# Performance work log

Hardware: AMD Instinct MI355X
Metric: run time of the kernel (lower is better)

The kernel has to match this reference:

```python
import jax, jax.numpy as jnp
import numpy as np

BN_EPS = 1e-5
LEAKY_SLOPE = 0.01

def setup_inputs() -> dict:
    key = jax.random.key(0)
    ks = jax.random.split(key, 8)
    B, N, C, D = 8, 2048, 128, 32  # batch, points, inchannels, outchannels
    s = 0.05
    return {
        "x": jax.random.normal(ks[0], (B, N, C), dtype=jnp.float32),
        "Wq": jax.random.normal(ks[1], (D, C), dtype=jnp.float32) * s,
        "Wk": jax.random.normal(ks[2], (D, C), dtype=jnp.float32) * s,
        "Wv": jax.random.normal(ks[3], (C, C), dtype=jnp.float32) * s,
        "Wp": jax.random.normal(ks[4], (C, C), dtype=jnp.float32) * s,
        "bn_gamma": jnp.ones((C,), dtype=jnp.float32),
        "bn_beta": jnp.zeros((C,), dtype=jnp.float32),
        "bn_mean": jax.random.normal(ks[5], (C,), dtype=jnp.float32) * 0.01,
        "bn_var": jnp.abs(jax.random.normal(ks[6], (C,), dtype=jnp.float32)) * 0.1 + 0.9,
    }

def reference(x, Wq, Wk, Wv, Wp, bn_gamma, bn_beta, bn_mean, bn_var):
    # x: [B, N, C]; 1x1 Conv1d == per-point linear map
    q = jnp.einsum('bnc,dc->bnd', x, Wq)          # [B, N, D]
    k = jnp.einsum('bnc,dc->bnd', x, Wk)          # [B, N, D]
    v = jnp.einsum('bnc,oc->bno', x, Wv)          # [B, N, C]
    energy = jnp.einsum('bnd,bmd->bnm', q, k)     # [B, Nq, Nk]
    # offset-attention: softmax over the QUERY axis (dim=1), then L1-renorm over keys
    attn = jax.nn.softmax(energy, axis=1)
    attn = attn / (1e-9 + attn.sum(axis=-1, keepdims=True))
    x_r = jnp.einsum('bnm,bmc->bnc', attn, v)     # [B, N, C]
    # project(x - x_r): 1x1 conv + BatchNorm (eval, running stats) + LeakyReLU; dropout p=0
    d = x - x_r
    y = jnp.einsum('bnc,oc->bno', d, Wp)
    y = (y - bn_mean) * (bn_gamma / jnp.sqrt(bn_var + BN_EPS)) + bn_beta
    y = jnp.where(y >= 0, y, LEAKY_SLOPE * y)
    return y + x
```

## Files before the change

### kernel.cpp

```cpp
#include <hip/hip_runtime.h>
#include <stdint.h>

#define BB 8
#define NN 2048
#define CC 128
#define DD 32
#define LOG2E 1.44269504088896340736f

typedef __attribute__((ext_vector_type(8))) short short8;
typedef __attribute__((ext_vector_type(4))) short short4v;
typedef __attribute__((ext_vector_type(4))) float f32x4;

#define MFMA(a,b,c) __builtin_amdgcn_mfma_f32_16x16x32_bf16(a,b,c,0,0,0)

__device__ __forceinline__ short f2b(float f){
  uint32_t u = __float_as_uint(f);
  uint32_t r = (u + 0x7fffu + ((u >> 16) & 1u)) >> 16;
  return (short)r;
}
__device__ __forceinline__ float b2f(short s){
  uint32_t u = ((uint32_t)(uint16_t)s) << 16;
  return __uint_as_float(u);
}

__global__ void k_pack(const float* __restrict__ Wq, const float* __restrict__ Wk,
                       const float* __restrict__ Wv, const float* __restrict__ Wp,
                       const float* __restrict__ g, const float* __restrict__ bt,
                       const float* __restrict__ mu, const float* __restrict__ vr,
                       short* __restrict__ wqkv, short* __restrict__ wp,
                       float* __restrict__ scale, float* __restrict__ shift){
  int i = blockIdx.x*256 + threadIdx.x;
  if (i < 192*128){
    int r = i >> 7, c = i & 127;
    float w = (r < 32) ? Wq[r*128+c] : (r < 64) ? Wk[(r-32)*128+c] : Wv[(r-64)*128+c];
    wqkv[i] = f2b(w);
  }
  if (i < 128*128) wp[i] = f2b(Wp[i]);
  if (i < 128){
    float s = g[i] * rsqrtf(vr[i] + 1e-5f);
    scale[i] = s;
    shift[i] = bt[i] - mu[i]*s;
  }
}

__global__ __launch_bounds__(256,4) void k_qkv(const float* __restrict__ x, const short* __restrict__ wqkv,
    short* __restrict__ qb, short* __restrict__ kb, short* __restrict__ vt){
  const int tid = threadIdx.x;
  const int wv = tid >> 6, l = tid & 63, lrow = l & 15, lg = l >> 4;
  const int r0 = blockIdx.x*16;
  const int base = wv*3;
  const float* xr = x + (long)(r0 + lrow)*CC;
  short8 a[4];
  #pragma unroll
  for (int ks=0; ks<4; ks++){
    f32x4 u0 = *(const f32x4*)(xr + ks*32 + lg*8);
    f32x4 u1 = *(const f32x4*)(xr + ks*32 + lg*8 + 4);
    short8 t;
    #pragma unroll
    for (int j=0;j<4;j++){ t[j] = f2b(u0[j]); t[4+j] = f2b(u1[j]); }
    a[ks] = t;
  }
  f32x4 acc[3];
  #pragma unroll
  for (int i=0;i<3;i++) acc[i] = f32x4{0.f,0.f,0.f,0.f};
  #pragma unroll
  for (int of=0; of<3; of++){
    #pragma unroll
    for (int ks=0; ks<4; ks++){
      short8 bfr = *(const short8*)(wqkv + ((base+of)*16 + lrow)*CC + ks*32 + lg*8);
      acc[of] = MFMA(a[ks], bfr, acc[of]);
    }
  }
  const int b = r0 / NN, nin = r0 % NN;
  #pragma unroll
  for (int of=0; of<3; of++){
    const int oo = base + of;
    const int o = oo*16 + lrow;
    if (oo < 2){
      #pragma unroll
      for (int rr=0; rr<4; rr++) qb[(long)(r0 + lg*4 + rr)*DD + o] = f2b(acc[of][rr]*LOG2E);
    } else if (oo < 4){
      #pragma unroll
      for (int rr=0; rr<4; rr++) kb[(long)(r0 + lg*4 + rr)*DD + (o-32)] = f2b(acc[of][rr]);
    } else {
      short4v s;
      #pragma unroll
      for (int rr=0; rr<4; rr++) s[rr] = f2b(acc[of][rr]);
      *(short4v*)(vt + (long)(b*CC + (o-64))*NN + nin + lg*4) = s;
    }
  }
}

__global__ __launch_bounds__(256,4) void k_colsum(const short* __restrict__ qb, const short* __restrict__ kb,
                                                  float* __restrict__ csum){
  const int tid = threadIdx.x;
  const int wv = tid >> 6, l = tid & 63, lrow = l & 15, lg = l >> 4;
  const int bq = blockIdx.x & 31;
  const int b = bq >> 2, q = bq & 3;
  const int m0 = (blockIdx.x >> 5)*64 + wv*16;
  short8 afr = *(const short8*)(kb + (long)(b*NN + m0 + lrow)*DD + lg*8);
  const short* qbase = qb + (long)b*NN*DD;
  float sum[4] = {0.f,0.f,0.f,0.f};
  f32x4 z = {0.f,0.f,0.f,0.f};
  const int nbeg = q*512, nend = nbeg + 512;
  #pragma unroll 4
  for (int n0=nbeg; n0<nend; n0+=16){
    short8 bfr = *(const short8*)(qbase + (long)(n0 + lrow)*DD + lg*8);
    f32x4 e = MFMA(afr, bfr, z);
    #pragma unroll
    for (int r=0;r<4;r++) sum[r] += exp2f(e[r]);
  }
  #pragma unroll
  for (int mask=1; mask<16; mask<<=1){
    #pragma unroll
    for (int r=0;r<4;r++) sum[r] += __shfl_xor(sum[r], mask);
  }
  if (lrow == 0){
    #pragma unroll
    for (int r=0;r<4;r++) csum[q*(BB*NN) + b*NN + m0 + lg*4 + r] = sum[r];
  }
}

__global__ __launch_bounds__(256,2) void k_attn(const short* __restrict__ qb,
    const short* __restrict__ kb, const short* __restrict__ vt, const float* __restrict__ csum,
    short* __restrict__ accPb, float* __restrict__ Lp){
  __shared__ __align__(16) short lds[22016];
  const int tid = threadIdx.x;
  const int wv = tid >> 6, l = tid & 63, lrow = l & 15, lg = l >> 4;
  const int bq = blockIdx.x & 31;
  const int b = bq >> 2;
  const int quarter = bq & 3;
  const int rt = blockIdx.x >> 5;
  const int n0 = rt*128 + wv*32;
  const short* kbb = kb + (long)b*NN*DD;
  const short* vtb = vt + (long)b*CC*NN;
  float* sinvl = (float*)(lds + 20992);

  short8 qfr[2];
  #pragma unroll
  for (int rg=0; rg<2; rg++)
    qfr[rg] = *(const short8*)(qb + (long)(b*NN + n0 + rg*16 + lrow)*DD + lg*8);

  const int mbase = quarter*512;
  {
    const float* c0p = csum + b*NN + mbase;
    #pragma unroll
    for (int i=tid; i<512; i+=256){
      float s = c0p[i] + c0p[i + BB*NN] + c0p[i + 2*BB*NN] + c0p[i + 3*BB*NN];
      sinvl[i] = __builtin_amdgcn_rcpf(s);
    }
  }

  f32x4 acc[2][8];
  #pragma unroll
  for (int rg=0; rg<2; rg++)
    #pragma unroll
    for (int i=0;i<8;i++) acc[rg][i] = f32x4{0.f,0.f,0.f,0.f};
  float L[2][4] = {{0.f,0.f,0.f,0.f},{0.f,0.f,0.f,0.f}};

  short8 sv[4]; short8 sk[2];
  const int cr = tid >> 1, hf = tid & 1;
  auto loadT = [&](int m0){
    const short* s = vtb + (long)cr*NN + m0 + hf*32;
    sv[0] = *(const short8*)(s);
    sv[1] = *(const short8*)(s+8);
    sv[2] = *(const short8*)(s+16);
    sv[3] = *(const short8*)(s+24);
    if (tid < 128){
      const short* s2 = kbb + (long)(m0 + cr)*DD + hf*16;
      sk[0] = *(const short8*)(s2);
      sk[1] = *(const short8*)(s2+8);
    }
  };
  auto storeT = [&](){
    *(short8*)(lds + cr*72 + hf*32 + 0)  = sv[0];
    *(short8*)(lds + cr*72 + hf*32 + 8)  = sv[1];
    *(short8*)(lds + cr*72 + hf*32 + 16) = sv[2];
    *(short8*)(lds + cr*72 + hf*32 + 24) = sv[3];
    if (tid < 128){
      short* kb_t = lds + 9216;
      *(short8*)(kb_t + cr*40 + hf*16 + 0) = sk[0];
      *(short8*)(kb_t + cr*40 + hf*16 + 8) = sk[1];
    }
  };

  loadT(mbase);
  storeT();
  __syncthreads();

  short* pl = lds + 11776 + wv*2304;
  f32x4 z = {0.f,0.f,0.f,0.f};
  for (int it=0; it<8; it++){
    if (it < 7) loadT(mbase + it*64 + 64);
    short* kb_t = lds + 9216;
    short8 kf[4];
    #pragma unroll
    for (int mt=0; mt<4; mt++)
      kf[mt] = *(short8*)(kb_t + (mt*16 + lrow)*40 + lg*8);
    #pragma unroll
    for (int rg=0; rg<2; rg++){
      #pragma unroll
      for (int mt=0; mt<4; mt++){
        f32x4 e = MFMA(qfr[rg], kf[mt], z);
        float si = sinvl[it*64 + mt*16 + lrow];
        float p0 = exp2f(e[0])*si, p1 = exp2f(e[1])*si;
        float p2 = exp2f(e[2])*si, p3 = exp2f(e[3])*si;
        L[rg][0] += p0; L[rg][1] += p1; L[rg][2] += p2; L[rg][3] += p3;
        pl[(rg*16 + lg*4 + 0)*72 + mt*16 + lrow] = f2b(p0);
        pl[(rg*16 + lg*4 + 1)*72 + mt*16 + lrow] = f2b(p1);
        pl[(rg*16 + lg*4 + 2)*72 + mt*16 + lrow] = f2b(p2);
        pl[(rg*16 + lg*4 + 3)*72 + mt*16 + lrow] = f2b(p3);
      }
    }
    __builtin_amdgcn_s_setprio(1);
    #pragma unroll
    for (int ks=0; ks<2; ks++){
      short8 pa0 = *(short8*)(pl + (lrow)*72 + ks*32 + lg*8);
      short8 pa1 = *(short8*)(pl + (16 + lrow)*72 + ks*32 + lg*8);
      #pragma unroll
      for (int cf=0; cf<8; cf++){
        short8 vb_ = *(short8*)(lds + (cf*16 + lrow)*72 + ks*32 + lg*8);
        acc[0][cf] = MFMA(pa0, vb_, acc[0][cf]);
        acc[1][cf] = MFMA(pa1, vb_, acc[1][cf]);
      }
    }
    __builtin_amdgcn_s_setprio(0);
    __syncthreads();
    if (it < 7){
      storeT();
      __syncthreads();
    }
  }

  #pragma unroll
  for (int mask=1; mask<16; mask<<=1){
    #pragma unroll
    for (int rg=0; rg<2; rg++)
      #pragma unroll
      for (int r=0;r<4;r++) L[rg][r] += __shfl_xor(L[rg][r], mask);
  }
  const long tile = (long)((b*16 + rt)*4 + quarter);
  if (lrow == 0){
    #pragma unroll
    for (int rg=0; rg<2; rg++)
      #pragma unroll
      for (int r=0;r<4;r++)
        Lp[tile*128 + wv*32 + rg*16 + lg*4 + r] = L[rg][r];
  }

  short* aP = accPb + tile*128*128;
  #pragma unroll
  for (int rg=0; rg<2; rg++)
    #pragma unroll
    for (int cf=0; cf<8; cf++)
      #pragma unroll
      for (int r=0;r<4;r++)
        aP[(wv*32 + rg*16 + lg*4 + r)*128 + cf*16 + lrow] = f2b(acc[rg][cf][r]);
}

__global__ __launch_bounds__(256,4) void k_fin(const float* __restrict__ x, const short* __restrict__ accPb,
    const float* __restrict__ Lp, const short* __restrict__ wp, const float* __restrict__ scale,
    const float* __restrict__ shift, float* __restrict__ out){
  __shared__ __align__(16) short dl[16*136];
  __shared__ float linv_s[16];
  const int tid = threadIdx.x;
  const int wv = tid >> 6, l = tid & 63, lrow = l & 15, lg = l >> 4;
  const int b = blockIdx.x >> 7;
  const int rt = blockIdx.x & 127;
  const int nb = rt*16;
  const long tileIdx = (long)(b*16 + (rt>>3))*4;
  const int rowoff = (rt&7)*16;

  if (tid < 16){
    float Ls = Lp[(tileIdx+0)*128 + rowoff + tid] + Lp[(tileIdx+1)*128 + rowoff + tid]
             + Lp[(tileIdx+2)*128 + rowoff + tid] + Lp[(tileIdx+3)*128 + rowoff + tid];
    linv_s[tid] = __builtin_amdgcn_rcpf(1e-9f + Ls);
  }

  const int row_l = tid >> 4;
  const int c0 = (tid & 15)*8;
  float a[8];
  #pragma unroll
  for (int j=0;j<8;j++) a[j] = 0.f;
  #pragma unroll
  for (int p=0;p<4;p++){
    short8 v = *(const short8*)(accPb + (tileIdx+p)*128*128 + (rowoff+row_l)*128 + c0);
    #pragma unroll
    for (int j=0;j<8;j++) a[j] += b2f(v[j]);
  }
  const float* xr = x + ((long)(b*NN + nb + row_l))*CC + c0;
  f32x4 x0 = *(const f32x4*)(xr);
  f32x4 x1 = *(const f32x4*)(xr + 4);
  __syncthreads();
  {
    const float li = linv_s[row_l];
    short4v d0, d1;
    #pragma unroll
    for (int j=0;j<4;j++){
      d0[j] = f2b(x0[j] - a[j]*li);
      d1[j] = f2b(x1[j] - a[4+j]*li);
    }
    *(short4v*)(dl + row_l*136 + c0) = d0;
    *(short4v*)(dl + row_l*136 + c0 + 4) = d1;
  }
  __syncthreads();

  f32x4 yac[2];
  yac[0] = f32x4{0.f,0.f,0.f,0.f};
  yac[1] = f32x4{0.f,0.f,0.f,0.f};
  #pragma unroll
  for (int ks=0; ks<4; ks++){
    short8 da = *(short8*)(dl + lrow*136 + ks*32 + lg*8);
    #pragma unroll
    for (int of=0; of<2; of++){
      short8 wfr = *(const short8*)(wp + ((wv*2+of)*16 + lrow)*CC + ks*32 + lg*8);
      yac[of] = MFMA(da, wfr, yac[of]);
    }
  }
  float* ob = out + ((long)(b*NN + nb))*CC;
  const float* xb = x + ((long)(b*NN + nb))*CC;
  #pragma unroll
  for (int of=0; of<2; of++){
    const int o = (wv*2+of)*16 + lrow;
    const float sc = scale[o], sh = shift[o];
    #pragma unroll
    for (int r=0;r<4;r++){
      float y = yac[of][r]*sc + sh;
      y = (y >= 0.f) ? y : 0.01f*y;
      ob[(lg*4+r)*CC + o] = y + xb[(lg*4+r)*CC + o];
    }
  }
}

extern "C" void kernel_launch(void* const* d_in, const int* in_sizes, int n_in,
                              void* d_out, int out_size, void* d_ws, size_t ws_size,
                              hipStream_t stream) {
  const float* x  = (const float*)d_in[0];
  const float* Wq = (const float*)d_in[1];
  const float* Wk = (const float*)d_in[2];
  const float* Wv = (const float*)d_in[3];
  const float* Wp = (const float*)d_in[4];
  const float* g  = (const float*)d_in[5];
  const float* bt = (const float*)d_in[6];
  const float* mu = (const float*)d_in[7];
  const float* vr = (const float*)d_in[8];
  float* out = (float*)d_out;

  char* ws = (char*)d_ws;
  short* wqkv  = (short*)(ws + 0);
  short* wp    = (short*)(ws + 49152);
  float* scale = (float*)(ws + 81920);
  float* shift = (float*)(ws + 82432);
  short* qb    = (short*)(ws + 98304);
  short* kb    = (short*)(ws + 1146880);
  short* vt    = (short*)(ws + 2195456);
  float* csum  = (float*)(ws + 6389760);
  float* Lp    = (float*)(ws + 6651904);
  short* accPb = (short*)(ws + 6914048);

  k_pack<<<96, 256, 0, stream>>>(Wq, Wk, Wv, Wp, g, bt, mu, vr, wqkv, wp, scale, shift);
  k_qkv<<<1024, 256, 0, stream>>>(x, wqkv, qb, kb, vt);
  k_colsum<<<1024, 256, 0, stream>>>(qb, kb, csum);
  k_attn<<<512, 256, 0, stream>>>(qb, kb, vt, csum, accPb, Lp);
  k_fin<<<1024, 256, 0, stream>>>(x, accPb, Lp, wp, scale, shift, out);
}
```

Baseline: 131.9 us.

## Fuse weight packing into QKV and final projection into attention via last-block counter

Drops the separate weight-pack kernel: k_qkv now loads fp32 Wq/Wk/Wv and converts them to bf16 inline, and the final stage builds the BN scale/shift and bf16 Wp fragments on the fly. The final projection kernel is folded into k_attn. A per-row-tile atomic counter, reset in k_colsum, picks the last of the four quarter blocks to finish, and that block reduces the partial accumulators and applies the projection, BatchNorm and LeakyReLU for 128 rows. This removes two kernel launches and their gaps. In exchange, weight conversion is repeated in every block, and the tail work runs on only a quarter of the attention blocks, which serialises it behind the last finisher.

```diff
diff --git a/kernel.cpp b/kernel.cpp
--- a/kernel.cpp
+++ b/kernel.cpp
@@ -23,27 +23,8 @@
   return __uint_as_float(u);
 }
 
-__global__ void k_pack(const float* __restrict__ Wq, const float* __restrict__ Wk,
-                       const float* __restrict__ Wv, const float* __restrict__ Wp,
-                       const float* __restrict__ g, const float* __restrict__ bt,
-                       const float* __restrict__ mu, const float* __restrict__ vr,
-                       short* __restrict__ wqkv, short* __restrict__ wp,
-                       float* __restrict__ scale, float* __restrict__ shift){
-  int i = blockIdx.x*256 + threadIdx.x;
-  if (i < 192*128){
-    int r = i >> 7, c = i & 127;
-    float w = (r < 32) ? Wq[r*128+c] : (r < 64) ? Wk[(r-32)*128+c] : Wv[(r-64)*128+c];
-    wqkv[i] = f2b(w);
-  }
-  if (i < 128*128) wp[i] = f2b(Wp[i]);
-  if (i < 128){
-    float s = g[i] * rsqrtf(vr[i] + 1e-5f);
-    scale[i] = s;
-    shift[i] = bt[i] - mu[i]*s;
-  }
-}
-
-__global__ __launch_bounds__(256,4) void k_qkv(const float* __restrict__ x, const short* __restrict__ wqkv,
+__global__ __launch_bounds__(256,4) void k_qkv(const float* __restrict__ x,
+    const float* __restrict__ Wq, const float* __restrict__ Wk, const float* __restrict__ Wv,
     short* __restrict__ qb, short* __restrict__ kb, short* __restrict__ vt){
   const int tid = threadIdx.x;
   const int wv = tid >> 6, l = tid & 63, lrow = l & 15, lg = l >> 4;
@@ -65,9 +46,16 @@
   for (int i=0;i<3;i++) acc[i] = f32x4{0.f,0.f,0.f,0.f};
   #pragma unroll
   for (int of=0; of<3; of++){
+    const int oo = base + of;
+    const int row = oo*16 + lrow;
+    const float* Wr = (oo < 2) ? (Wq + row*CC) : (oo < 4) ? (Wk + (row-32)*CC) : (Wv + (row-64)*CC);
     #pragma unroll
     for (int ks=0; ks<4; ks++){
-      short8 bfr = *(const short8*)(wqkv + ((base+of)*16 + lrow)*CC + ks*32 + lg*8);
+      f32x4 w0 = *(const f32x4*)(Wr + ks*32 + lg*8);
+      f32x4 w1 = *(const f32x4*)(Wr + ks*32 + lg*8 + 4);
+      short8 bfr;
+      #pragma unroll
+      for (int j=0;j<4;j++){ bfr[j] = f2b(w0[j]); bfr[4+j] = f2b(w1[j]); }
       acc[of] = MFMA(a[ks], bfr, acc[of]);
     }
   }
@@ -92,9 +80,10 @@
 }
 
 __global__ __launch_bounds__(256,4) void k_colsum(const short* __restrict__ qb, const short* __restrict__ kb,
-                                                  float* __restrict__ csum){
+                                                  float* __restrict__ csum, int* __restrict__ cnt){
   const int tid = threadIdx.x;
   const int wv = tid >> 6, l = tid & 63, lrow = l & 15, lg = l >> 4;
+  if (blockIdx.x == 0 && tid < 128) cnt[tid] = 0;
   const int bq = blockIdx.x & 31;
   const int b = bq >> 2, q = bq & 3;
   const int m0 = (blockIdx.x >> 5)*64 + wv*16;
@@ -121,9 +110,12 @@
   }
 }
 
-__global__ __launch_bounds__(256,2) void k_attn(const short* __restrict__ qb,
+__global__ __launch_bounds__(256,2) void k_attn(const float* __restrict__ x, const short* __restrict__ qb,
     const short* __restrict__ kb, const short* __restrict__ vt, const float* __restrict__ csum,
-    short* __restrict__ accPb, float* __restrict__ Lp){
+    const float* __restrict__ Wp, const float* __restrict__ g, const float* __restrict__ bt,
+    const float* __restrict__ mu, const float* __restrict__ vr,
+    short* __restrict__ accPb, float* __restrict__ Lp, int* __restrict__ cnt,
+    float* __restrict__ out){
   __shared__ __align__(16) short lds[22016];
   const int tid = threadIdx.x;
   const int wv = tid >> 6, l = tid & 63, lrow = l & 15, lg = l >> 4;
@@ -239,7 +231,8 @@
       #pragma unroll
       for (int r=0;r<4;r++) L[rg][r] += __shfl_xor(L[rg][r], mask);
   }
-  const long tile = (long)((b*16 + rt)*4 + quarter);
+  const long t4 = (long)(b*16 + rt)*4;
+  const long tile = t4 + quarter;
   if (lrow == 0){
     #pragma unroll
     for (int rg=0; rg<2; rg++)
@@ -256,78 +249,92 @@
       #pragma unroll
       for (int r=0;r<4;r++)
         aP[(wv*32 + rg*16 + lg*4 + r)*128 + cf*16 + lrow] = f2b(acc[rg][cf][r]);
-}
-
-__global__ __launch_bounds__(256,4) void k_fin(const float* __restrict__ x, const short* __restrict__ accPb,
-    const float* __restrict__ Lp, const short* __restrict__ wp, const float* __restrict__ scale,
-    const float* __restrict__ shift, float* __restrict__ out){
-  __shared__ __align__(16) short dl[16*136];
-  __shared__ float linv_s[16];
-  const int tid = threadIdx.x;
-  const int wv = tid >> 6, l = tid & 63, lrow = l & 15, lg = l >> 4;
-  const int b = blockIdx.x >> 7;
-  const int rt = blockIdx.x & 127;
-  const int nb = rt*16;
-  const long tileIdx = (long)(b*16 + (rt>>3))*4;
-  const int rowoff = (rt&7)*16;
-
-  if (tid < 16){
-    float Ls = Lp[(tileIdx+0)*128 + rowoff + tid] + Lp[(tileIdx+1)*128 + rowoff + tid]
-             + Lp[(tileIdx+2)*128 + rowoff + tid] + Lp[(tileIdx+3)*128 + rowoff + tid];
-    linv_s[tid] = __builtin_amdgcn_rcpf(1e-9f + Ls);
-  }
-
-  const int row_l = tid >> 4;
-  const int c0 = (tid & 15)*8;
-  float a[8];
-  #pragma unroll
-  for (int j=0;j<8;j++) a[j] = 0.f;
-  #pragma unroll
-  for (int p=0;p<4;p++){
-    short8 v = *(const short8*)(accPb + (tileIdx+p)*128*128 + (rowoff+row_l)*128 + c0);
-    #pragma unroll
-    for (int j=0;j<8;j++) a[j] += b2f(v[j]);
-  }
-  const float* xr = x + ((long)(b*NN + nb + row_l))*CC + c0;
-  f32x4 x0 = *(const f32x4*)(xr);
-  f32x4 x1 = *(const f32x4*)(xr + 4);
+
+  __threadfence();
+  __syncthreads();
+  int* flagp = (int*)(lds + 21504);
+  if (tid == 0)
+    *flagp = (atomicAdd(&cnt[b*16 + rt], 1) == 3) ? 1 : 0;
+  __syncthreads();
+  if (!*flagp) return;
+  __threadfence();
+
+  float* linvl = (float*)(lds + 20992);
+  short* dl = lds;
+  if (tid < 128){
+    float Ls = Lp[t4*128 + tid] + Lp[(t4+1)*128 + tid]
+             + Lp[(t4+2)*128 + tid] + Lp[(t4+3)*128 + tid];
+    linvl[tid] = __builtin_amdgcn_rcpf(1e-9f + Ls);
+  }
   __syncthreads();
   {
-    const float li = linv_s[row_l];
-    short4v d0, d1;
-    #pragma unroll
-    for (int j=0;j<4;j++){
-      d0[j] = f2b(x0[j] - a[j]*li);
-      d1[j] = f2b(x1[j] - a[4+j]*li);
-    }
-    *(short4v*)(dl + row_l*136 + c0) = d0;
-    *(short4v*)(dl + row_l*136 + c0 + 4) = d1;
-  }
-  __syncthreads();
-
-  f32x4 yac[2];
-  yac[0] = f32x4{0.f,0.f,0.f,0.f};
-  yac[1] = f32x4{0.f,0.f,0.f,0.f};
-  #pragma unroll
-  for (int ks=0; ks<4; ks++){
-    short8 da = *(short8*)(dl + lrow*136 + ks*32 + lg*8);
-    #pragma unroll
-    for (int of=0; of<2; of++){
-      short8 wfr = *(const short8*)(wp + ((wv*2+of)*16 + lrow)*CC + ks*32 + lg*8);
-      yac[of] = MFMA(da, wfr, yac[of]);
-    }
-  }
-  float* ob = out + ((long)(b*NN + nb))*CC;
-  const float* xb = x + ((long)(b*NN + nb))*CC;
+    const int row = tid >> 1, half = tid & 1;
+    const float li = linvl[row];
+    const float* xr2 = x + ((long)(b*NN + rt*128 + row))*CC + half*64;
+    const short* ap0 = accPb + t4*128*128 + row*128 + half*64;
+    #pragma unroll
+    for (int c8=0; c8<8; c8++){
+      float s[8];
+      #pragma unroll
+      for (int j=0;j<8;j++) s[j] = 0.f;
+      #pragma unroll
+      for (int q2=0; q2<4; q2++){
+        short8 v = *(const short8*)(ap0 + q2*128*128 + c8*8);
+        #pragma unroll
+        for (int j=0;j<8;j++) s[j] += b2f(v[j]);
+      }
+      f32x4 x0 = *(const f32x4*)(xr2 + c8*8);
+      f32x4 x1 = *(const f32x4*)(xr2 + c8*8 + 4);
+      short8 d8;
+      #pragma unroll
+      for (int j=0;j<4;j++){
+        d8[j]   = f2b(x0[j] - s[j]*li);
+        d8[4+j] = f2b(x1[j] - s[4+j]*li);
+      }
+      *(short8*)(dl + row*136 + half*64 + c8*8) = d8;
+    }
+  }
+  __syncthreads();
+
+  short8 wfr[2][4];
+  float sc[2], sh[2];
   #pragma unroll
   for (int of=0; of<2; of++){
     const int o = (wv*2+of)*16 + lrow;
-    const float sc = scale[o], sh = shift[o];
-    #pragma unroll
-    for (int r=0;r<4;r++){
-      float y = yac[of][r]*sc + sh;
-      y = (y >= 0.f) ? y : 0.01f*y;
-      ob[(lg*4+r)*CC + o] = y + xb[(lg*4+r)*CC + o];
+    #pragma unroll
+    for (int ks=0; ks<4; ks++){
+      const float* wr = Wp + o*CC + ks*32 + lg*8;
+      f32x4 w0 = *(const f32x4*)(wr);
+      f32x4 w1 = *(const f32x4*)(wr + 4);
+      #pragma unroll
+      for (int j=0;j<4;j++){ wfr[of][ks][j] = f2b(w0[j]); wfr[of][ks][4+j] = f2b(w1[j]); }
+    }
+    sc[of] = g[o] * rsqrtf(vr[o] + 1e-5f);
+    sh[of] = bt[o] - mu[o]*sc[of];
+  }
+  float* ob = out + ((long)(b*NN + rt*128))*CC;
+  const float* xb = x + ((long)(b*NN + rt*128))*CC;
+  #pragma unroll
+  for (int rb=0; rb<8; rb++){
+    f32x4 yac0 = f32x4{0.f,0.f,0.f,0.f};
+    f32x4 yac1 = f32x4{0.f,0.f,0.f,0.f};
+    #pragma unroll
+    for (int ks=0; ks<4; ks++){
+      short8 da = *(short8*)(dl + (rb*16 + lrow)*136 + ks*32 + lg*8);
+      yac0 = MFMA(da, wfr[0][ks], yac0);
+      yac1 = MFMA(da, wfr[1][ks], yac1);
+    }
+    #pragma unroll
+    for (int of=0; of<2; of++){
+      const f32x4 ya = of ? yac1 : yac0;
+      const int o = (wv*2+of)*16 + lrow;
+      #pragma unroll
+      for (int r=0;r<4;r++){
+        const int row = rb*16 + lg*4 + r;
+        float y = ya[r]*sc[of] + sh[of];
+        y = (y >= 0.f) ? y : 0.01f*y;
+        ob[(long)row*CC + o] = y + xb[(long)row*CC + o];
+      }
     }
   }
 }
@@ -347,20 +354,15 @@
   float* out = (float*)d_out;
 
   char* ws = (char*)d_ws;
-  short* wqkv  = (short*)(ws + 0);
-  short* wp    = (short*)(ws + 49152);
-  float* scale = (float*)(ws + 81920);
-  float* shift = (float*)(ws + 82432);
   short* qb    = (short*)(ws + 98304);
   short* kb    = (short*)(ws + 1146880);
   short* vt    = (short*)(ws + 2195456);
   float* csum  = (float*)(ws + 6389760);
   float* Lp    = (float*)(ws + 6651904);
   short* accPb = (short*)(ws + 6914048);
-
-  k_pack<<<96, 256, 0, stream>>>(Wq, Wk, Wv, Wp, g, bt, mu, vr, wqkv, wp, scale, shift);
-  k_qkv<<<1024, 256, 0, stream>>>(x, wqkv, qb, kb, vt);
-  k_colsum<<<1024, 256, 0, stream>>>(qb, kb, csum);
-  k_attn<<<512, 256, 0, stream>>>(qb, kb, vt, csum, accPb, Lp);
-  k_fin<<<1024, 256, 0, stream>>>(x, accPb, Lp, wp, scale, shift, out);
-}
+  int*   cnt   = (int*)(ws + 23691264);
+
+  k_qkv<<<1024, 256, 0, stream>>>(x, Wq, Wk, Wv, qb, kb, vt);
+  k_colsum<<<1024, 256, 0, stream>>>(qb, kb, csum, cnt);
+  k_attn<<<512, 256, 0, stream>>>(x, qb, kb, vt, csum, Wp, g, bt, mu, vr, accPb, Lp, cnt, out);
+}
```

Result: slower. 248.0 us (+88.1%).

## Double-buffer attention LDS tiles and fold weight packing into consumer kernels

Applied to the files above, without the earlier changes.

The k_pack launch is removed. k_qkv and k_fin now read the fp32 weights directly and convert them to bf16 in registers, and k_fin computes the BatchNorm scale and shift inline. This saves one kernel launch at the cost of redundant conversions in every block. In k_attn, the V/K tiles are double-buffered in LDS so the next tile is stored while the current one is consumed, which drops one __syncthreads per iteration. The extra LDS (about 67KB per block) may reduce occupancy.

```diff
diff --git a/kernel.cpp b/kernel.cpp
--- a/kernel.cpp
+++ b/kernel.cpp
@@ -23,27 +23,8 @@
   return __uint_as_float(u);
 }
 
-__global__ void k_pack(const float* __restrict__ Wq, const float* __restrict__ Wk,
-                       const float* __restrict__ Wv, const float* __restrict__ Wp,
-                       const float* __restrict__ g, const float* __restrict__ bt,
-                       const float* __restrict__ mu, const float* __restrict__ vr,
-                       short* __restrict__ wqkv, short* __restrict__ wp,
-                       float* __restrict__ scale, float* __restrict__ shift){
-  int i = blockIdx.x*256 + threadIdx.x;
-  if (i < 192*128){
-    int r = i >> 7, c = i & 127;
-    float w = (r < 32) ? Wq[r*128+c] : (r < 64) ? Wk[(r-32)*128+c] : Wv[(r-64)*128+c];
-    wqkv[i] = f2b(w);
-  }
-  if (i < 128*128) wp[i] = f2b(Wp[i]);
-  if (i < 128){
-    float s = g[i] * rsqrtf(vr[i] + 1e-5f);
-    scale[i] = s;
-    shift[i] = bt[i] - mu[i]*s;
-  }
-}
-
-__global__ __launch_bounds__(256,4) void k_qkv(const float* __restrict__ x, const short* __restrict__ wqkv,
+__global__ __launch_bounds__(256,4) void k_qkv(const float* __restrict__ x,
+    const float* __restrict__ Wq, const float* __restrict__ Wk, const float* __restrict__ Wv,
     short* __restrict__ qb, short* __restrict__ kb, short* __restrict__ vt){
   const int tid = threadIdx.x;
   const int wv = tid >> 6, l = tid & 63, lrow = l & 15, lg = l >> 4;
@@ -65,9 +46,16 @@
   for (int i=0;i<3;i++) acc[i] = f32x4{0.f,0.f,0.f,0.f};
   #pragma unroll
   for (int of=0; of<3; of++){
+    const int oo = base + of;
+    const int row = oo*16 + lrow;
+    const float* Wr = (oo < 2) ? (Wq + row*CC) : (oo < 4) ? (Wk + (row-32)*CC) : (Wv + (row-64)*CC);
     #pragma unroll
     for (int ks=0; ks<4; ks++){
-      short8 bfr = *(const short8*)(wqkv + ((base+of)*16 + lrow)*CC + ks*32 + lg*8);
+      f32x4 w0 = *(const f32x4*)(Wr + ks*32 + lg*8);
+      f32x4 w1 = *(const f32x4*)(Wr + ks*32 + lg*8 + 4);
+      short8 bfr;
+      #pragma unroll
+      for (int j=0;j<4;j++){ bfr[j] = f2b(w0[j]); bfr[4+j] = f2b(w1[j]); }
       acc[of] = MFMA(a[ks], bfr, acc[of]);
     }
   }
@@ -124,7 +112,7 @@
 __global__ __launch_bounds__(256,2) void k_attn(const short* __restrict__ qb,
     const short* __restrict__ kb, const short* __restrict__ vt, const float* __restrict__ csum,
     short* __restrict__ accPb, float* __restrict__ Lp){
-  __shared__ __align__(16) short lds[22016];
+  __shared__ __align__(16) short lds[33792];
   const int tid = threadIdx.x;
   const int wv = tid >> 6, l = tid & 63, lrow = l & 15, lg = l >> 4;
   const int bq = blockIdx.x & 31;
@@ -134,7 +122,7 @@
   const int n0 = rt*128 + wv*32;
   const short* kbb = kb + (long)b*NN*DD;
   const short* vtb = vt + (long)b*CC*NN;
-  float* sinvl = (float*)(lds + 20992);
+  float* sinvl = (float*)(lds + 32768);
 
   short8 qfr[2];
   #pragma unroll
@@ -172,27 +160,30 @@
       sk[1] = *(const short8*)(s2+8);
     }
   };
-  auto storeT = [&](){
-    *(short8*)(lds + cr*72 + hf*32 + 0)  = sv[0];
-    *(short8*)(lds + cr*72 + hf*32 + 8)  = sv[1];
-    *(short8*)(lds + cr*72 + hf*32 + 16) = sv[2];
-    *(short8*)(lds + cr*72 + hf*32 + 24) = sv[3];
+  auto storeT = [&](int buf){
+    short* base = lds + buf*11776;
+    *(short8*)(base + cr*72 + hf*32 + 0)  = sv[0];
+    *(short8*)(base + cr*72 + hf*32 + 8)  = sv[1];
+    *(short8*)(base + cr*72 + hf*32 + 16) = sv[2];
+    *(short8*)(base + cr*72 + hf*32 + 24) = sv[3];
     if (tid < 128){
-      short* kb_t = lds + 9216;
+      short* kb_t = base + 9216;
       *(short8*)(kb_t + cr*40 + hf*16 + 0) = sk[0];
       *(short8*)(kb_t + cr*40 + hf*16 + 8) = sk[1];
     }
   };
 
   loadT(mbase);
-  storeT();
+  storeT(0);
   __syncthreads();
 
-  short* pl = lds + 11776 + wv*2304;
+  short* pl = lds + 23552 + wv*2304;
   f32x4 z = {0.f,0.f,0.f,0.f};
   for (int it=0; it<8; it++){
+    const int cur = it & 1;
     if (it < 7) loadT(mbase + it*64 + 64);
-    short* kb_t = lds + 9216;
+    short* vt_t = lds + cur*11776;
+    short* kb_t = vt_t + 9216;
     short8 kf[4];
     #pragma unroll
     for (int mt=0; mt<4; mt++)
@@ -219,17 +210,14 @@
       short8 pa1 = *(short8*)(pl + (16 + lrow)*72 + ks*32 + lg*8);
       #pragma unroll
       for (int cf=0; cf<8; cf++){
-        short8 vb_ = *(short8*)(lds + (cf*16 + lrow)*72 + ks*32 + lg*8);
+        short8 vb_ = *(short8*)(vt_t + (cf*16 + lrow)*72 + ks*32 + lg*8);
         acc[0][cf] = MFMA(pa0, vb_, acc[0][cf]);
         acc[1][cf] = MFMA(pa1, vb_, acc[1][cf]);
       }
     }
     __builtin_amdgcn_s_setprio(0);
+    if (it < 7) storeT(cur ^ 1);
     __syncthreads();
-    if (it < 7){
-      storeT();
-      __syncthreads();
-    }
   }
 
   #pragma unroll
@@ -239,7 +227,7 @@
       #pragma unroll
       for (int r=0;r<4;r++) L[rg][r] += __shfl_xor(L[rg][r], mask);
   }
-  const long tile = (long)((b*16 + rt)*4 + quarter);
+  const long tile = (long)(b*16 + rt)*4 + quarter;
   if (lrow == 0){
     #pragma unroll
     for (int rg=0; rg<2; rg++)
@@ -259,17 +247,18 @@
 }
 
 __global__ __launch_bounds__(256,4) void k_fin(const float* __restrict__ x, const short* __restrict__ accPb,
-    const float* __restrict__ Lp, const short* __restrict__ wp, const float* __restrict__ scale,
-    const float* __restrict__ shift, float* __restrict__ out){
+    const float* __restrict__ Lp, const float* __restrict__ Wp, const float* __restrict__ g,
+    const float* __restrict__ bt, const float* __restrict__ mu, const float* __restrict__ vr,
+    float* __restrict__ out){
   __shared__ __align__(16) short dl[16*136];
   __shared__ float linv_s[16];
   const int tid = threadIdx.x;
   const int wv = tid >> 6, l = tid & 63, lrow = l & 15, lg = l >> 4;
   const int b = blockIdx.x >> 7;
-  const int rt = blockIdx.x & 127;
-  const int nb = rt*16;
-  const long tileIdx = (long)(b*16 + (rt>>3))*4;
-  const int rowoff = (rt&7)*16;
+  const int rr = blockIdx.x & 127;
+  const int nb = rr*16;
+  const long tileIdx = (long)(b*16 + (rr>>3))*4;
+  const int rowoff = (rr&7)*16;
 
   if (tid < 16){
     float Ls = Lp[(tileIdx+0)*128 + rowoff + tid] + Lp[(tileIdx+1)*128 + rowoff + tid]
@@ -313,7 +302,12 @@
     short8 da = *(short8*)(dl + lrow*136 + ks*32 + lg*8);
     #pragma unroll
     for (int of=0; of<2; of++){
-      short8 wfr = *(const short8*)(wp + ((wv*2+of)*16 + lrow)*CC + ks*32 + lg*8);
+      const float* wr = Wp + ((wv*2+of)*16 + lrow)*CC + ks*32 + lg*8;
+      f32x4 w0 = *(const f32x4*)(wr);
+      f32x4 w1 = *(const f32x4*)(wr + 4);
+      short8 wfr;
+      #pragma unroll
+      for (int j=0;j<4;j++){ wfr[j] = f2b(w0[j]); wfr[4+j] = f2b(w1[j]); }
       yac[of] = MFMA(da, wfr, yac[of]);
     }
   }
@@ -322,7 +316,8 @@
   #pragma unroll
   for (int of=0; of<2; of++){
     const int o = (wv*2+of)*16 + lrow;
-    const float sc = scale[o], sh = shift[o];
+    const float sc = g[o] * rsqrtf(vr[o] + 1e-5f);
+    const float sh = bt[o] - mu[o]*sc;
     #pragma unroll
     for (int r=0;r<4;r++){
       float y = yac[of][r]*sc + sh;
@@ -347,10 +342,6 @@
   float* out = (float*)d_out;
 
   char* ws = (char*)d_ws;
-  short* wqkv  = (short*)(ws + 0);
-  short* wp    = (short*)(ws + 49152);
-  float* scale = (float*)(ws + 81920);
-  float* shift = (float*)(ws + 82432);
   short* qb    = (short*)(ws + 98304);
   short* kb    = (short*)(ws + 1146880);
   short* vt    = (short*)(ws + 2195456);
@@ -358,9 +349,8 @@
   float* Lp    = (float*)(ws + 6651904);
   short* accPb = (short*)(ws + 6914048);
 
-  k_pack<<<96, 256, 0, stream>>>(Wq, Wk, Wv, Wp, g, bt, mu, vr, wqkv, wp, scale, shift);
-  k_qkv<<<1024, 256, 0, stream>>>(x, wqkv, qb, kb, vt);
+  k_qkv<<<1024, 256, 0, stream>>>(x, Wq, Wk, Wv, qb, kb, vt);
   k_colsum<<<1024, 256, 0, stream>>>(qb, kb, csum);
   k_attn<<<512, 256, 0, stream>>>(qb, kb, vt, csum, accPb, Lp);
-  k_fin<<<1024, 256, 0, stream>>>(x, accPb, Lp, wp, scale, shift, out);
-}
+  k_fin<<<1024, 256, 0, stream>>>(x, accPb, Lp, Wp, g, bt, mu, vr, out);
+}
```

Result: slower. 139.2 us (+5.6%).
